# Optimization experiments

Hardware: AMD Instinct MI355X
Metric: run time of the kernel (lower is better)

Reference implementation:

```python
import jax, jax.numpy as jnp
import numpy as np

C = 256  # channels
SHAPES = [(8, C, 80, 80), (8, C, 40, 40), (8, C, 20, 20), (8, C, 10, 10)]
EPS = 1e-8  # torch cosine_similarity eps


def _nearest_resize(x, H, W):
    # Matches F.interpolate(mode='nearest'): src_idx = floor(dst_idx * in/out)
    b, c, h, w = x.shape
    rows = (jnp.arange(H) * h) // H
    cols = (jnp.arange(W) * w) // W
    return x[:, :, rows[:, None], cols[None, :]]


def setup_inputs() -> dict:
    key = jax.random.key(0)
    ks = jax.random.split(key, 12)
    d = {}
    for i, s in enumerate(SHAPES):
        d[f"f{i}"] = jax.random.normal(ks[i], s, dtype=jnp.float32)
        d[f"w{i}"] = jax.random.normal(ks[4 + i], (C, C), dtype=jnp.float32) / jnp.sqrt(jnp.float32(C))
        d[f"b{i}"] = jax.random.normal(ks[8 + i], (C,), dtype=jnp.float32) * 0.01
    return d


def reference(f0, f1, f2, f3, w0, w1, w2, w3, b0, b1, b2, b3):
    feats = [f0, f1, f2, f3]
    ws = [w0, w1, w2, w3]
    bs = [b0, b1, b2, b3]
    H = max(f.shape[2] for f in feats)
    W = max(f.shape[3] for f in feats)
    proj = []
    for f, w, b in zip(feats, ws, bs):
        # 1x1 conv == per-pixel GEMM over channels
        p = jnp.einsum('bchw,oc->bohw', f, w) + b[None, :, None, None]
        if p.shape[2] != H or p.shape[3] != W:
            p = _nearest_resize(p, H, W)
        proj.append(p)
    B = proj[0].shape[0]
    N = len(proj)
    x = jnp.stack(proj, axis=1).reshape(B, N, C, H * W)  # [B,N,C,L]
    # Pairwise cosine similarity along channel dim at each spatial location,
    # then mean over locations (vectorized form of the O(N^2) torch loop).
    dot = jnp.einsum('bicl,bjcl->bijl', x, x)            # [B,N,N,L]
    nrm = jnp.sqrt(jnp.einsum('bicl,bicl->bil', x, x))   # [B,N,L]
    denom = jnp.maximum(nrm[:, :, None, :] * nrm[:, None, :, :], EPS)
    attn = (dot / denom).mean(axis=-1)                   # [B,N,N]
    return jax.nn.softmax(attn, axis=-1)
```

## Files before the change

kernel.cpp:

```cpp
#include <hip/hip_runtime.h>


#define CCH 256
#define WPITCH 40

typedef __attribute__((ext_vector_type(8))) short short8;
typedef __attribute__((ext_vector_type(4))) short short4_;
typedef __attribute__((ext_vector_type(4))) float float4_;

__device__ inline short f2bf(float x) {
    union { float f; unsigned u; } c; c.f = x;
    unsigned u = c.u + 0x7FFFu + ((c.u >> 16) & 1u);
    return (short)(u >> 16);
}
__device__ inline float bf2f(short b) {
    union { unsigned u; float f; } c; c.u = ((unsigned)(unsigned short)b) << 16;
    return c.f;
}

__global__ __launch_bounds__(256) void proj_small(
    const float* __restrict__ f1, const float* __restrict__ f2,
    const float* __restrict__ f3,
    const float* __restrict__ w1, const float* __restrict__ w2,
    const float* __restrict__ w3,
    const float* __restrict__ b1, const float* __restrict__ b2,
    const float* __restrict__ b3,
    short* __restrict__ u1, short* __restrict__ u2, short* __restrict__ u3)
{
    __shared__ __align__(16) short Wt[256 * WPITCH];
    __shared__ __align__(16) short Ft[64 * WPITCH];

    const int blk = blockIdx.x;
    int b, tile, L;
    const float* F; const float* Wg; const float* bias; short* U;
    if (blk < 200)      { int r = blk;       b = r / 25; tile = r % 25; L = 1600; F = f1; Wg = w1; bias = b1; U = u1; }
    else if (blk < 256) { int r = blk - 200; b = r / 7;  tile = r % 7;  L = 400;  F = f2; Wg = w2; bias = b2; U = u2; }
    else                { int r = blk - 256; b = r / 2;  tile = r % 2;  L = 100;  F = f3; Wg = w3; bias = b3; U = u3; }

    const int t    = threadIdx.x;
    const int lane = t & 63;
    const int wav  = t >> 6;
    const int ln   = lane & 15;
    const int quad = lane >> 4;
    const int pixbase = tile * 64;
    const float* Fb = F + (size_t)b * CCH * L;

    const int wo = t >> 2;
    const int wk = (t & 3) * 8;
    const int fpix = t & 63;
    const int fchunk = t >> 6;
    const int gpix0 = pixbase + fpix;
    const bool pin = gpix0 < L;
    const int gl0 = pin ? gpix0 : 0;

    float4_ wbufA[4], wbufB[4];
    float fbuf[8];
    auto loadW = [&](int ks) {
#pragma unroll
        for (int p = 0; p < 4; ++p) {
            const float* srcp = Wg + (size_t)(p * 64 + wo) * CCH + ks * 32 + wk;
            wbufA[p] = *(const float4_*)srcp;
            wbufB[p] = *(const float4_*)(srcp + 4);
        }
    };
    auto loadF = [&](int ks) {
        const float* fs = Fb + (size_t)(ks * 32 + fchunk * 8) * L + gl0;
#pragma unroll
        for (int j = 0; j < 8; ++j) fbuf[j] = fs[(size_t)j * L];
    };

    float4_ acc[16];
#pragma unroll
    for (int i = 0; i < 16; ++i) acc[i] = (float4_){0.f, 0.f, 0.f, 0.f};

    loadW(0); loadF(0);
    for (int ks = 0; ks < 8; ++ks) {
        __syncthreads();
#pragma unroll
        for (int p = 0; p < 4; ++p) {
            short8 v;
#pragma unroll
            for (int e = 0; e < 4; ++e) { v[e] = f2bf(wbufA[p][e]); v[e + 4] = f2bf(wbufB[p][e]); }
            *(short8*)(&Wt[(p * 64 + wo) * WPITCH + wk]) = v;
        }
        {
            short8 v;
#pragma unroll
            for (int j = 0; j < 8; ++j) v[j] = pin ? f2bf(fbuf[j]) : (short)0;
            *(short8*)(&Ft[fpix * WPITCH + fchunk * 8]) = v;
        }
        __syncthreads();
        const int ksn = (ks + 1) & 7;
        loadW(ksn); loadF(ksn);

        short8 bfrag = *(const short8*)(&Ft[(wav * 16 + ln) * WPITCH + quad * 8]);
#pragma unroll
        for (int mt = 0; mt < 16; ++mt) {
            short8 afrag = *(const short8*)(&Wt[(mt * 16 + ln) * WPITCH + quad * 8]);
            acc[mt] = __builtin_amdgcn_mfma_f32_16x16x32_bf16(afrag, bfrag, acc[mt], 0, 0, 0);
        }
    }

    float ss = 0.f;
#pragma unroll
    for (int mt = 0; mt < 16; ++mt) {
        float4_ bv = *(const float4_*)(bias + mt * 16 + quad * 4);
#pragma unroll
        for (int r = 0; r < 4; ++r) { float v = acc[mt][r] + bv[r]; acc[mt][r] = v; ss += v * v; }
    }
    ss += __shfl_xor(ss, 16);
    ss += __shfl_xor(ss, 32);
    const float inv = 1.f / sqrtf(fmaxf(ss, 1e-24f));

    const int gpixw = pixbase + wav * 16 + ln;
    if (gpixw < L) {
        short* dst = U + ((size_t)b * L + gpixw) * CCH;
#pragma unroll
        for (int mt = 0; mt < 16; ++mt) {
            short4_ v;
#pragma unroll
            for (int r = 0; r < 4; ++r) v[r] = f2bf(acc[mt][r] * inv);
            *(short4_*)(dst + mt * 16 + quad * 4) = v;
        }
    }
}

__global__ __launch_bounds__(256) void proj0_dots(
    const float* __restrict__ F, const float* __restrict__ Wg,
    const float* __restrict__ bias,
    const short* __restrict__ u1, const short* __restrict__ u2,
    const short* __restrict__ u3,
    float* __restrict__ partial)
{
    __shared__ __align__(16) short Wt[256 * WPITCH];
    __shared__ __align__(16) short Ft[64 * WPITCH];
    short* S1 = Wt;
    short* S2 = Wt + 4096;
    short* S3 = Wt + 5120;
    __shared__ float red[4][3];
    __shared__ float redB[3];

    const int c3 = blockIdx.x;
    const int b  = blockIdx.y;
    const int H3 = c3 / 10, W3 = c3 - H3 * 10;

    const int t    = threadIdx.x;
    const int lane = t & 63;
    const int wav  = t >> 6;
    const int ln   = lane & 15;
    const int quad = lane >> 4;
    const float* Fb = F + (size_t)b * CCH * 6400;

    const int wo = t >> 2;
    const int wk = (t & 3) * 8;
    const int fpix = t & 63;
    const int fchunk = t >> 6;
    const int gl = (8 * H3 + (fpix >> 3)) * 80 + 8 * W3 + (fpix & 7);

    float4_ wbufA[4], wbufB[4];
    float fbuf[8];
    auto loadW = [&](int ks) {
#pragma unroll
        for (int p = 0; p < 4; ++p) {
            const float* srcp = Wg + (size_t)(p * 64 + wo) * CCH + ks * 32 + wk;
            wbufA[p] = *(const float4_*)srcp;
            wbufB[p] = *(const float4_*)(srcp + 4);
        }
    };
    auto loadF = [&](int ks) {
        const float* fs = Fb + (size_t)(ks * 32 + fchunk * 8) * 6400 + gl;
#pragma unroll
        for (int j = 0; j < 8; ++j) fbuf[j] = fs[(size_t)j * 6400];
    };

    float4_ acc[16];
#pragma unroll
    for (int i = 0; i < 16; ++i) acc[i] = (float4_){0.f, 0.f, 0.f, 0.f};

    loadW(0); loadF(0);
    for (int ks = 0; ks < 8; ++ks) {
        __syncthreads();
#pragma unroll
        for (int p = 0; p < 4; ++p) {
            short8 v;
#pragma unroll
            for (int e = 0; e < 4; ++e) { v[e] = f2bf(wbufA[p][e]); v[e + 4] = f2bf(wbufB[p][e]); }
            *(short8*)(&Wt[(p * 64 + wo) * WPITCH + wk]) = v;
        }
        {
            short8 v;
#pragma unroll
            for (int j = 0; j < 8; ++j) v[j] = f2bf(fbuf[j]);
            *(short8*)(&Ft[fpix * WPITCH + fchunk * 8]) = v;
        }
        __syncthreads();
        const int ksn = (ks + 1) & 7;
        loadW(ksn); loadF(ksn);

        short8 bfrag = *(const short8*)(&Ft[(wav * 16 + ln) * WPITCH + quad * 8]);
#pragma unroll
        for (int mt = 0; mt < 16; ++mt) {
            short8 afrag = *(const short8*)(&Wt[(mt * 16 + ln) * WPITCH + quad * 8]);
            acc[mt] = __builtin_amdgcn_mfma_f32_16x16x32_bf16(afrag, bfrag, acc[mt], 0, 0, 0);
        }
    }

    float ss = 0.f;
#pragma unroll
    for (int mt = 0; mt < 16; ++mt) {
        float4_ bv = *(const float4_*)(bias + mt * 16 + quad * 4);
#pragma unroll
        for (int r = 0; r < 4; ++r) { float v = acc[mt][r] + bv[r]; acc[mt][r] = v; ss += v * v; }
    }
    ss += __shfl_xor(ss, 16);
    ss += __shfl_xor(ss, 32);
    const float inv = 1.f / sqrtf(fmaxf(ss, 1e-24f));

    __syncthreads();

    {
        const int p1 = t >> 4, ck = (t & 15) * 16;
        const int h1 = p1 >> 2, w1 = p1 & 3;
        const short* src = u1 + ((size_t)(b * 1600 + (4 * H3 + h1) * 40 + 4 * W3 + w1)) * CCH + ck;
        *(short8*)(&S1[p1 * 256 + ck])     = *(const short8*)src;
        *(short8*)(&S1[p1 * 256 + ck + 8]) = *(const short8*)(src + 8);
    }
    if (t < 64) {
        const int p2 = t >> 4, ck = (t & 15) * 16;
        const int h2 = p2 >> 1, w2 = p2 & 1;
        const short* src = u2 + ((size_t)(b * 400 + (2 * H3 + h2) * 20 + 2 * W3 + w2)) * CCH + ck;
        *(short8*)(&S2[p2 * 256 + ck])     = *(const short8*)src;
        *(short8*)(&S2[p2 * 256 + ck + 8]) = *(const short8*)(src + 8);
    }
    if (t < 16) {
        const int ck = t * 16;
        const short* src = u3 + ((size_t)(b * 100 + H3 * 10 + W3)) * CCH + ck;
        *(short8*)(&S3[ck])     = *(const short8*)src;
        *(short8*)(&S3[ck + 8]) = *(const short8*)(src + 8);
    }
    __syncthreads();

    const int pme = wav * 16 + ln;
    const int ph = pme >> 3, pw = pme & 7;
    const int c1 = (ph >> 1) * 4 + (pw >> 1);
    const int c2 = (ph >> 2) * 2 + (pw >> 2);
    float d01 = 0.f, d02 = 0.f, d03 = 0.f;
#pragma unroll
    for (int mt = 0; mt < 16; ++mt) {
        const int ch = mt * 16 + quad * 4;
        short4_ v1 = *(const short4_*)(&S1[c1 * 256 + ch]);
        short4_ v2 = *(const short4_*)(&S2[c2 * 256 + ch]);
        short4_ v3 = *(const short4_*)(&S3[ch]);
#pragma unroll
        for (int r = 0; r < 4; ++r) {
            float a = acc[mt][r] * inv;
            d01 += a * bf2f(v1[r]);
            d02 += a * bf2f(v2[r]);
            d03 += a * bf2f(v3[r]);
        }
    }
    float vals[3] = {d01, d02, d03};
#pragma unroll
    for (int p = 0; p < 3; ++p) {
        float v = vals[p];
        v += __shfl_xor(v, 1);  v += __shfl_xor(v, 2);  v += __shfl_xor(v, 4);
        v += __shfl_xor(v, 8);  v += __shfl_xor(v, 16); v += __shfl_xor(v, 32);
        if (lane == 0) red[wav][p] = v;
    }

    if (wav == 0) {
        float e12 = 0.f, e13 = 0.f, e23 = 0.f;
        {
            const int cc1 = lane >> 2, q = lane & 3;
            const int cc2 = ((cc1 >> 2) >> 1) * 2 + ((cc1 & 3) >> 1);
#pragma unroll
            for (int k = 0; k < 16; ++k) {
                short4_ a1 = *(const short4_*)(&S1[cc1 * 256 + q * 64 + k * 4]);
                short4_ a2 = *(const short4_*)(&S2[cc2 * 256 + q * 64 + k * 4]);
                short4_ a3 = *(const short4_*)(&S3[q * 64 + k * 4]);
#pragma unroll
                for (int r = 0; r < 4; ++r) {
                    float x1 = bf2f(a1[r]);
                    e12 += x1 * bf2f(a2[r]);
                    e13 += x1 * bf2f(a3[r]);
                }
            }
        }
        if (lane < 16) {
            const int dc2 = lane >> 2, dq = lane & 3;
#pragma unroll
            for (int k = 0; k < 16; ++k) {
                short4_ a2 = *(const short4_*)(&S2[dc2 * 256 + dq * 64 + k * 4]);
                short4_ a3 = *(const short4_*)(&S3[dq * 64 + k * 4]);
#pragma unroll
                for (int r = 0; r < 4; ++r) e23 += bf2f(a2[r]) * bf2f(a3[r]);
            }
        }
        float evals[3] = {e12, e13, e23};
#pragma unroll
        for (int p = 0; p < 3; ++p) {
            float v = evals[p];
            v += __shfl_xor(v, 1);  v += __shfl_xor(v, 2);  v += __shfl_xor(v, 4);
            v += __shfl_xor(v, 8);  v += __shfl_xor(v, 16); v += __shfl_xor(v, 32);
            if (lane == 0) redB[p] = v;
        }
    }
    __syncthreads();
    if (t < 3)
        partial[((size_t)b * 6 + t) * 100 + c3] = red[0][t] + red[1][t] + red[2][t] + red[3][t];
    else if (t < 6)
        partial[((size_t)b * 6 + t) * 100 + c3] = redB[t - 3];
}

__global__ void softmax4(const float* __restrict__ partial, float* __restrict__ out) {
    int t = threadIdx.x;
    if (t >= 128) return;
    int b = t >> 4, i = (t >> 2) & 3, j = t & 3;
    float a[4];
#pragma unroll
    for (int jj = 0; jj < 4; ++jj) {
        if (jj == i) { a[jj] = 1.0f; continue; }
        int lo = i < jj ? i : jj;
        int hi = i < jj ? jj : i;
        int pidx;
        if (lo == 0) pidx = hi - 1;
        else if (lo == 1) pidx = 1 + hi;
        else pidx = 5;
        const float* pp = partial + ((size_t)b * 6 + pidx) * 100;
        float s = 0.f;
        for (int k = 0; k < 100; ++k) s += pp[k];
        int rf = 80 >> lo;
        a[jj] = s / (float)(rf * rf);
    }
    float m = fmaxf(fmaxf(a[0], a[1]), fmaxf(a[2], a[3]));
    float e0 = expf(a[0] - m), e1 = expf(a[1] - m), e2 = expf(a[2] - m), e3 = expf(a[3] - m);
    float sum = e0 + e1 + e2 + e3;
    float ev = (j == 0) ? e0 : (j == 1) ? e1 : (j == 2) ? e2 : e3;
    out[t] = ev / sum;
}

extern "C" void kernel_launch(void* const* d_in, const int* in_sizes, int n_in,
                              void* d_out, int out_size, void* d_ws, size_t ws_size,
                              hipStream_t stream) {
    const float* f[4]  = {(const float*)d_in[0], (const float*)d_in[3],
                          (const float*)d_in[6], (const float*)d_in[9]};
    const float* w[4]  = {(const float*)d_in[1], (const float*)d_in[4],
                          (const float*)d_in[7], (const float*)d_in[10]};
    const float* bs[4] = {(const float*)d_in[2], (const float*)d_in[5],
                          (const float*)d_in[8], (const float*)d_in[11]};

    char* ws = (char*)d_ws;
    size_t off = 0;
    short* u1 = (short*)(ws + off); off += (size_t)8 * CCH * 1600 * sizeof(short);
    short* u2 = (short*)(ws + off); off += (size_t)8 * CCH * 400  * sizeof(short);
    short* u3 = (short*)(ws + off); off += (size_t)8 * CCH * 100  * sizeof(short);
    float* partial = (float*)(ws + off);

    proj_small<<<272, 256, 0, stream>>>(f[1], f[2], f[3],
                                        w[1], w[2], w[3],
                                        bs[1], bs[2], bs[3],
                                        u1, u2, u3);

    proj0_dots<<<dim3(100, 8), 256, 0, stream>>>(f[0], w[0], bs[0],
                                                 u1, u2, u3, partial);

    softmax4<<<1, 128, 0, stream>>>(partial, (float*)d_out);
}
```

Measured before the change: 167.7 us.

## Prepack w0 to bf16 fragments and DMA tiles directly into LDS with double buffering

```diff
diff --git a/kernel.cpp b/kernel.cpp
--- a/kernel.cpp
+++ b/kernel.cpp
@@ -18,26 +18,49 @@
     return c.f;
 }
 
+__device__ inline void dma16(const void* g, void* l) {
+    __builtin_amdgcn_global_load_lds(
+        (const __attribute__((address_space(1))) void*)g,
+        (__attribute__((address_space(3))) void*)l, 16, 0, 0);
+}
+
 __global__ __launch_bounds__(256) void proj_small(
     const float* __restrict__ f1, const float* __restrict__ f2,
     const float* __restrict__ f3,
-    const float* __restrict__ w1, const float* __restrict__ w2,
-    const float* __restrict__ w3,
+    const float* __restrict__ w0, const float* __restrict__ w1,
+    const float* __restrict__ w2, const float* __restrict__ w3,
     const float* __restrict__ b1, const float* __restrict__ b2,
     const float* __restrict__ b3,
-    short* __restrict__ u1, short* __restrict__ u2, short* __restrict__ u3)
+    short* __restrict__ u1, short* __restrict__ u2, short* __restrict__ u3,
+    short* __restrict__ wp)
 {
     __shared__ __align__(16) short Wt[256 * WPITCH];
     __shared__ __align__(16) short Ft[64 * WPITCH];
 
     const int blk = blockIdx.x;
+    const int t = threadIdx.x;
+
+    if (blk >= 272) {
+        int id = (blk - 272) * 256 + t;
+        int ks = id >> 10;
+        int rest = id & 1023;
+        int mt = rest >> 6;
+        int fl = rest & 63;
+        int ln = fl & 15, qd = fl >> 4;
+        const float* src = w0 + (size_t)(mt * 16 + ln) * CCH + ks * 32 + qd * 8;
+        short8 v;
+#pragma unroll
+        for (int j = 0; j < 8; ++j) v[j] = f2bf(src[j]);
+        *(short8*)(wp + (size_t)id * 8) = v;
+        return;
+    }
+
     int b, tile, L;
     const float* F; const float* Wg; const float* bias; short* U;
     if (blk < 200)      { int r = blk;       b = r / 25; tile = r % 25; L = 1600; F = f1; Wg = w1; bias = b1; U = u1; }
     else if (blk < 256) { int r = blk - 200; b = r / 7;  tile = r % 7;  L = 400;  F = f2; Wg = w2; bias = b2; U = u2; }
     else                { int r = blk - 256; b = r / 2;  tile = r % 2;  L = 100;  F = f3; Wg = w3; bias = b3; U = u3; }
 
-    const int t    = threadIdx.x;
     const int lane = t & 63;
     const int wav  = t >> 6;
     const int ln   = lane & 15;
@@ -125,82 +148,75 @@
     }
 }
 
-__global__ __launch_bounds__(256) void proj0_dots(
-    const float* __restrict__ F, const float* __restrict__ Wg,
+__global__ __launch_bounds__(512) void proj0_dots(
+    const float* __restrict__ F, const short* __restrict__ wp,
     const float* __restrict__ bias,
     const short* __restrict__ u1, const short* __restrict__ u2,
     const short* __restrict__ u3,
     float* __restrict__ partial)
 {
-    __shared__ __align__(16) short Wt[256 * WPITCH];
-    __shared__ __align__(16) short Ft[64 * WPITCH];
-    short* S1 = Wt;
-    short* S2 = Wt + 4096;
-    short* S3 = Wt + 5120;
-    __shared__ float red[4][3];
-    __shared__ float redB[3];
-
-    const int c3 = blockIdx.x;
+    __shared__ __align__(16) char smem[65536];
+    short* Wb0 = (short*)smem;
+    short* Wb1 = (short*)(smem + 16384);
+    float* Fb0 = (float*)(smem + 32768);
+    float* Fb1 = (float*)(smem + 49152);
+    short* S1 = (short*)smem;
+    short* S2 = (short*)(smem + 16384);
+    short* S3 = (short*)(smem + 20480);
+    float* redF = (float*)(smem + 24576);
+    float* redC = (float*)(smem + 24576 + 96);
+
+    const int c  = blockIdx.x;
     const int b  = blockIdx.y;
-    const int H3 = c3 / 10, W3 = c3 - H3 * 10;
-
-    const int t    = threadIdx.x;
+    const int R  = c / 5, C = c - R * 5;
+    const int t  = threadIdx.x;
     const int lane = t & 63;
     const int wav  = t >> 6;
     const int ln   = lane & 15;
     const int quad = lane >> 4;
-    const float* Fb = F + (size_t)b * CCH * 6400;
-
-    const int wo = t >> 2;
-    const int wk = (t & 3) * 8;
-    const int fpix = t & 63;
-    const int fchunk = t >> 6;
-    const int gl = (8 * H3 + (fpix >> 3)) * 80 + 8 * W3 + (fpix & 7);
-
-    float4_ wbufA[4], wbufB[4];
-    float fbuf[8];
-    auto loadW = [&](int ks) {
-#pragma unroll
-        for (int p = 0; p < 4; ++p) {
-            const float* srcp = Wg + (size_t)(p * 64 + wo) * CCH + ks * 32 + wk;
-            wbufA[p] = *(const float4_*)srcp;
-            wbufB[p] = *(const float4_*)(srcp + 4);
+    const float* Fbase = F + (size_t)b * CCH * 6400;
+
+    auto dmaW = [&](int ks, int buf) {
+        short* Wb = buf ? Wb1 : Wb0;
+#pragma unroll
+        for (int m = 0; m < 2; ++m) {
+            const int k = wav * 2 + m;
+            const short* g = wp + (size_t)ks * 8192 + k * 512 + lane * 8;
+            dma16(g, Wb + k * 512);
         }
     };
-    auto loadF = [&](int ks) {
-        const float* fs = Fb + (size_t)(ks * 32 + fchunk * 8) * 6400 + gl;
-#pragma unroll
-        for (int j = 0; j < 8; ++j) fbuf[j] = fs[(size_t)j * 6400];
+    auto dmaF = [&](int ks, int buf) {
+        float* Fb = buf ? Fb1 : Fb0;
+#pragma unroll
+        for (int m = 0; m < 2; ++m) {
+            const int k = wav * 2 + m;
+            const int chl = 2 * k + (lane >> 5);
+            const int px4 = (lane & 31) * 4;
+            const int gpx = (8 * R + (px4 >> 4)) * 80 + 16 * C + (px4 & 15);
+            const float* g = Fbase + (size_t)(ks * 32 + chl) * 6400 + gpx;
+            dma16(g, Fb + k * 256);
+        }
     };
 
     float4_ acc[16];
 #pragma unroll
     for (int i = 0; i < 16; ++i) acc[i] = (float4_){0.f, 0.f, 0.f, 0.f};
 
-    loadW(0); loadF(0);
+    const int pxme = wav * 16 + ln;
+
+    dmaW(0, 0); dmaF(0, 0);
     for (int ks = 0; ks < 8; ++ks) {
         __syncthreads();
-#pragma unroll
-        for (int p = 0; p < 4; ++p) {
-            short8 v;
-#pragma unroll
-            for (int e = 0; e < 4; ++e) { v[e] = f2bf(wbufA[p][e]); v[e + 4] = f2bf(wbufB[p][e]); }
-            *(short8*)(&Wt[(p * 64 + wo) * WPITCH + wk]) = v;
-        }
-        {
-            short8 v;
-#pragma unroll
-            for (int j = 0; j < 8; ++j) v[j] = f2bf(fbuf[j]);
-            *(short8*)(&Ft[fpix * WPITCH + fchunk * 8]) = v;
-        }
-        __syncthreads();
-        const int ksn = (ks + 1) & 7;
-        loadW(ksn); loadF(ksn);
-
-        short8 bfrag = *(const short8*)(&Ft[(wav * 16 + ln) * WPITCH + quad * 8]);
+        if (ks < 7) { dmaW(ks + 1, (ks + 1) & 1); dmaF(ks + 1, (ks + 1) & 1); }
+        const short* Wl = (ks & 1) ? Wb1 : Wb0;
+        const float* Fl = (ks & 1) ? Fb1 : Fb0;
+        short8 bfrag;
+#pragma unroll
+        for (int j = 0; j < 8; ++j)
+            bfrag[j] = f2bf(Fl[(quad * 8 + j) * 128 + pxme]);
 #pragma unroll
         for (int mt = 0; mt < 16; ++mt) {
-            short8 afrag = *(const short8*)(&Wt[(mt * 16 + ln) * WPITCH + quad * 8]);
+            short8 afrag = *(const short8*)(Wl + mt * 512 + lane * 8);
             acc[mt] = __builtin_amdgcn_mfma_f32_16x16x32_bf16(afrag, bfrag, acc[mt], 0, 0, 0);
         }
     }
@@ -220,37 +236,37 @@
 
     {
         const int p1 = t >> 4, ck = (t & 15) * 16;
-        const int h1 = p1 >> 2, w1 = p1 & 3;
-        const short* src = u1 + ((size_t)(b * 1600 + (4 * H3 + h1) * 40 + 4 * W3 + w1)) * CCH + ck;
+        const int lr = p1 >> 3, lc = p1 & 7;
+        const short* src = u1 + ((size_t)(b * 1600 + (4 * R + lr) * 40 + 8 * C + lc)) * CCH + ck;
         *(short8*)(&S1[p1 * 256 + ck])     = *(const short8*)src;
         *(short8*)(&S1[p1 * 256 + ck + 8]) = *(const short8*)(src + 8);
     }
-    if (t < 64) {
+    if (t < 128) {
         const int p2 = t >> 4, ck = (t & 15) * 16;
-        const int h2 = p2 >> 1, w2 = p2 & 1;
-        const short* src = u2 + ((size_t)(b * 400 + (2 * H3 + h2) * 20 + 2 * W3 + w2)) * CCH + ck;
+        const int lr = p2 >> 2, lc = p2 & 3;
+        const short* src = u2 + ((size_t)(b * 400 + (2 * R + lr) * 20 + 4 * C + lc)) * CCH + ck;
         *(short8*)(&S2[p2 * 256 + ck])     = *(const short8*)src;
         *(short8*)(&S2[p2 * 256 + ck + 8]) = *(const short8*)(src + 8);
     }
-    if (t < 16) {
-        const int ck = t * 16;
-        const short* src = u3 + ((size_t)(b * 100 + H3 * 10 + W3)) * CCH + ck;
-        *(short8*)(&S3[ck])     = *(const short8*)src;
-        *(short8*)(&S3[ck + 8]) = *(const short8*)(src + 8);
+    if (t < 32) {
+        const int p3 = t >> 4, ck = (t & 15) * 16;
+        const short* src = u3 + ((size_t)(b * 100 + R * 10 + 2 * C + p3)) * CCH + ck;
+        *(short8*)(&S3[p3 * 256 + ck])     = *(const short8*)src;
+        *(short8*)(&S3[p3 * 256 + ck + 8]) = *(const short8*)(src + 8);
     }
     __syncthreads();
 
-    const int pme = wav * 16 + ln;
-    const int ph = pme >> 3, pw = pme & 7;
-    const int c1 = (ph >> 1) * 4 + (pw >> 1);
-    const int c2 = (ph >> 2) * 2 + (pw >> 2);
+    const int pr = pxme >> 4, pc = pxme & 15;
+    const int c1l = (pr >> 1) * 8 + (pc >> 1);
+    const int c2l = (pr >> 2) * 4 + (pc >> 2);
+    const int c3l = pc >> 3;
     float d01 = 0.f, d02 = 0.f, d03 = 0.f;
 #pragma unroll
     for (int mt = 0; mt < 16; ++mt) {
         const int ch = mt * 16 + quad * 4;
-        short4_ v1 = *(const short4_*)(&S1[c1 * 256 + ch]);
-        short4_ v2 = *(const short4_*)(&S2[c2 * 256 + ch]);
-        short4_ v3 = *(const short4_*)(&S3[ch]);
+        short4_ v1 = *(const short4_*)(&S1[c1l * 256 + ch]);
+        short4_ v2 = *(const short4_*)(&S2[c2l * 256 + ch]);
+        short4_ v3 = *(const short4_*)(&S3[c3l * 256 + ch]);
 #pragma unroll
         for (int r = 0; r < 4; ++r) {
             float a = acc[mt][r] * inv;
@@ -259,57 +275,75 @@
             d03 += a * bf2f(v3[r]);
         }
     }
-    float vals[3] = {d01, d02, d03};
-#pragma unroll
-    for (int p = 0; p < 3; ++p) {
-        float v = vals[p];
-        v += __shfl_xor(v, 1);  v += __shfl_xor(v, 2);  v += __shfl_xor(v, 4);
-        v += __shfl_xor(v, 8);  v += __shfl_xor(v, 16); v += __shfl_xor(v, 32);
-        if (lane == 0) red[wav][p] = v;
-    }
-
-    if (wav == 0) {
-        float e12 = 0.f, e13 = 0.f, e23 = 0.f;
-        {
-            const int cc1 = lane >> 2, q = lane & 3;
-            const int cc2 = ((cc1 >> 2) >> 1) * 2 + ((cc1 & 3) >> 1);
+    {
+        float vals[3] = {d01, d02, d03};
+#pragma unroll
+        for (int p = 0; p < 3; ++p) {
+            float v = vals[p];
+            v += __shfl_xor(v, 1);  v += __shfl_xor(v, 2);  v += __shfl_xor(v, 4);
+            v += __shfl_xor(v, 8);  v += __shfl_xor(v, 16); v += __shfl_xor(v, 32);
+            if (lane == 0) redF[wav * 3 + p] = v;
+        }
+    }
+
+    if (wav < 2) {
+        const int p1 = wav * 16 + (lane >> 2);
+        const int q  = lane & 3;
+        const int lr = p1 >> 3, lc = p1 & 7;
+        const int par2 = (lr >> 1) * 4 + (lc >> 1);
+        const int par3 = lc >> 2;
+        float e12 = 0.f, e13 = 0.f;
+#pragma unroll
+        for (int k = 0; k < 16; ++k) {
+            short4_ a1 = *(const short4_*)(&S1[p1 * 256 + q * 64 + k * 4]);
+            short4_ a2 = *(const short4_*)(&S2[par2 * 256 + q * 64 + k * 4]);
+            short4_ a3 = *(const short4_*)(&S3[par3 * 256 + q * 64 + k * 4]);
+#pragma unroll
+            for (int r = 0; r < 4; ++r) {
+                float x1 = bf2f(a1[r]);
+                e12 += x1 * bf2f(a2[r]);
+                e13 += x1 * bf2f(a3[r]);
+            }
+        }
+        float ev[2] = {e12, e13};
+#pragma unroll
+        for (int p = 0; p < 2; ++p) {
+            float v = ev[p];
+            v += __shfl_xor(v, 1);  v += __shfl_xor(v, 2);  v += __shfl_xor(v, 4);
+            v += __shfl_xor(v, 8);  v += __shfl_xor(v, 16); v += __shfl_xor(v, 32);
+            if (lane == 0) redC[wav * 2 + p] = v;
+        }
+    } else if (wav == 2) {
+        float e23 = 0.f;
+        if (lane < 32) {
+            const int p2 = lane >> 2;
+            const int q  = lane & 3;
+            const int par3 = (p2 & 3) >> 1;
 #pragma unroll
             for (int k = 0; k < 16; ++k) {
-                short4_ a1 = *(const short4_*)(&S1[cc1 * 256 + q * 64 + k * 4]);
-                short4_ a2 = *(const short4_*)(&S2[cc2 * 256 + q * 64 + k * 4]);
-                short4_ a3 = *(const short4_*)(&S3[q * 64 + k * 4]);
-#pragma unroll
-                for (int r = 0; r < 4; ++r) {
-                    float x1 = bf2f(a1[r]);
-                    e12 += x1 * bf2f(a2[r]);
-                    e13 += x1 * bf2f(a3[r]);
-                }
-            }
-        }
-        if (lane < 16) {
-            const int dc2 = lane >> 2, dq = lane & 3;
-#pragma unroll
-            for (int k = 0; k < 16; ++k) {
-                short4_ a2 = *(const short4_*)(&S2[dc2 * 256 + dq * 64 + k * 4]);
-                short4_ a3 = *(const short4_*)(&S3[dq * 64 + k * 4]);
+                short4_ a2 = *(const short4_*)(&S2[p2 * 256 + q * 64 + k * 4]);
+                short4_ a3 = *(const short4_*)(&S3[par3 * 256 + q * 64 + k * 4]);
 #pragma unroll
                 for (int r = 0; r < 4; ++r) e23 += bf2f(a2[r]) * bf2f(a3[r]);
             }
         }
-        float evals[3] = {e12, e13, e23};
-#pragma unroll
-        for (int p = 0; p < 3; ++p) {
-            float v = evals[p];
-            v += __shfl_xor(v, 1);  v += __shfl_xor(v, 2);  v += __shfl_xor(v, 4);
-            v += __shfl_xor(v, 8);  v += __shfl_xor(v, 16); v += __shfl_xor(v, 32);
-            if (lane == 0) redB[p] = v;
-        }
+        e23 += __shfl_xor(e23, 1);  e23 += __shfl_xor(e23, 2);  e23 += __shfl_xor(e23, 4);
+        e23 += __shfl_xor(e23, 8);  e23 += __shfl_xor(e23, 16); e23 += __shfl_xor(e23, 32);
+        if (lane == 0) redC[4] = e23;
     }
     __syncthreads();
-    if (t < 3)
-        partial[((size_t)b * 6 + t) * 100 + c3] = red[0][t] + red[1][t] + red[2][t] + red[3][t];
-    else if (t < 6)
-        partial[((size_t)b * 6 + t) * 100 + c3] = redB[t - 3];
+
+    if (t < 6) {
+        float v;
+        if (t < 3) {
+            v = 0.f;
+#pragma unroll
+            for (int w = 0; w < 8; ++w) v += redF[w * 3 + t];
+        } else if (t == 3) v = redC[0] + redC[2];
+        else if (t == 4)   v = redC[1] + redC[3];
+        else               v = redC[4];
+        partial[((size_t)b * 6 + t) * 50 + c] = v;
+    }
 }
 
 __global__ void softmax4(const float* __restrict__ partial, float* __restrict__ out) {
@@ -326,9 +360,9 @@
         if (lo == 0) pidx = hi - 1;
         else if (lo == 1) pidx = 1 + hi;
         else pidx = 5;
-        const float* pp = partial + ((size_t)b * 6 + pidx) * 100;
+        const float* pp = partial + ((size_t)b * 6 + pidx) * 50;
         float s = 0.f;
-        for (int k = 0; k < 100; ++k) s += pp[k];
+        for (int k = 0; k < 50; ++k) s += pp[k];
         int rf = 80 >> lo;
         a[jj] = s / (float)(rf * rf);
     }
@@ -354,15 +388,16 @@
     short* u1 = (short*)(ws + off); off += (size_t)8 * CCH * 1600 * sizeof(short);
     short* u2 = (short*)(ws + off); off += (size_t)8 * CCH * 400  * sizeof(short);
     short* u3 = (short*)(ws + off); off += (size_t)8 * CCH * 100  * sizeof(short);
+    short* wp = (short*)(ws + off); off += (size_t)65536 * sizeof(short);
     float* partial = (float*)(ws + off);
 
-    proj_small<<<272, 256, 0, stream>>>(f[1], f[2], f[3],
-                                        w[1], w[2], w[3],
+    proj_small<<<304, 256, 0, stream>>>(f[1], f[2], f[3],
+                                        w[0], w[1], w[2], w[3],
                                         bs[1], bs[2], bs[3],
-                                        u1, u2, u3);
-
-    proj0_dots<<<dim3(100, 8), 256, 0, stream>>>(f[0], w[0], bs[0],
-                                                 u1, u2, u3, partial);
+                                        u1, u2, u3, wp);
+
+    proj0_dots<<<dim3(50, 8), 512, 0, stream>>>(f[0], wp, bs[0],
+                                                u1, u2, u3, partial);
 
     softmax4<<<1, 128, 0, stream>>>(partial, (float*)d_out);
 }
```

Measured after the change: 159.3 us. 1.05x faster.
